# Performance work log

Hardware: AMD Instinct MI355X
Metric: run time of the kernel (lower is better)

Reference implementation:

```python
import jax, jax.numpy as jnp
import numpy as np

N_QUBITS = 16
N_LAYERS = 3
DIM = 1 << N_QUBITS  # 65536 statevector amplitudes

# Bit i of a basis index corresponds to wire i, wire 0 = most significant bit
# (PennyLane default.qubit convention).
_idx = np.arange(DIM)
_shifts = np.arange(N_QUBITS - 1, -1, -1)
_BITS_NP = (_idx[:, None] >> _shifts[None, :]) & 1  # [DIM, N_QUBITS]
# CNOT chain (i -> i+1) applied sequentially makes new bit_i = XOR(bit_0..bit_i)
_y = (np.bitwise_xor.accumulate(_BITS_NP, axis=1) * (1 << _shifts)).sum(axis=1)
_inv = np.empty(DIM, np.int64)
_inv[_y] = _idx  # state_new = state_old[INV_PERM]
INV_PERM = jnp.asarray(_inv)
SIGNS = jnp.asarray(1.0 - 2.0 * _BITS_NP, dtype=jnp.float32)  # [DIM, N_QUBITS], PauliZ eigenvalues


def _circuit(theta, qw):
    """Batched 16-qubit statevector sim. theta: [B, 16] RY angles, qw: [3, 16] RZ angles.
    Returns [B, 16] PauliZ expectation values."""
    B = theta.shape[0]
    c = jnp.cos(theta * 0.5)
    s = jnp.sin(theta * 0.5)
    # RY(theta)|0> = cos(t/2)|0> + sin(t/2)|1>; product state via repeated Kronecker
    state = jnp.ones((B, 1), jnp.complex64)
    for i in range(N_QUBITS):
        q = jnp.stack([c[:, i], s[:, i]], axis=-1).astype(jnp.complex64)  # [B, 2]
        state = (state[:, :, None] * q[:, None, :]).reshape(B, -1)
    for l in range(N_LAYERS):
        # RZ(phi) = diag(e^{-i phi/2}, e^{+i phi/2}); combined diagonal over all qubits
        diag = jnp.ones((1,), jnp.complex64)
        for i in range(N_QUBITS):
            ph = jnp.exp(1j * qw[l, i] * jnp.array([-0.5, 0.5], jnp.float32))  # complex64
            diag = (diag[:, None] * ph[None, :]).reshape(-1)
        state = (state * diag[None, :])[:, INV_PERM]  # RZ layer then CNOT chain permutation
    probs = state.real ** 2 + state.imag ** 2  # [B, DIM]
    return probs @ SIGNS  # [B, 16]


def setup_inputs() -> dict:
    key = jax.random.key(0)
    k = jax.random.split(key, 6)
    B, D = 512, 128
    x = jax.random.normal(k[0], (B, D), jnp.float32)
    w_in = jax.random.normal(k[1], (N_QUBITS, D), jnp.float32) * (1.0 / np.sqrt(D))
    b_in = jax.random.normal(k[2], (N_QUBITS,), jnp.float32) * 0.01
    # TorchLayer default init: uniform in [0, 2*pi]
    q_weights = jax.random.uniform(k[3], (N_LAYERS, N_QUBITS), jnp.float32, 0.0, 2.0 * np.pi)
    w_out = jax.random.normal(k[4], (D, N_QUBITS), jnp.float32) * (1.0 / np.sqrt(N_QUBITS))
    b_out = jax.random.normal(k[5], (D,), jnp.float32) * 0.01
    return {"x": x, "w_in": w_in, "b_in": b_in, "q_weights": q_weights,
            "w_out": w_out, "b_out": b_out}


def reference(x, w_in, b_in, q_weights, w_out, b_out):
    h = x @ w_in.T + b_in  # [B, 16]
    h = jax.lax.stop_gradient(h)  # original does x.detach() before the quantum layer
    ev = _circuit(h, q_weights)  # [B, 16]
    return ev @ w_out.T + b_out  # [B, 128]
```

## Files before the change

### kernel.cpp

```cpp
#include <hip/hip_runtime.h>
#include <hip/hip_bf16.h>


#define NQ 16
#define D  128

__global__ __launch_bounds__(128) void qlayer_kernel(
    const float* __restrict__ x,
    const float* __restrict__ w_in,
    const float* __restrict__ b_in,
    const float* __restrict__ w_out,
    const float* __restrict__ b_out,
    float* __restrict__ out)
{
    __shared__ float s_x[D];
    __shared__ float s_part[D];
    __shared__ float s_cos[NQ];
    __shared__ float s_ev[NQ];

    const int b = blockIdx.x;
    const int t = threadIdx.x;

    s_x[t] = x[b * D + t];
    __syncthreads();

    const int i = t >> 3;
    const int j = t & 7;
    const int d0 = j * 16;
    float p = 0.f;
#pragma unroll
    for (int d = 0; d < 16; ++d)
        p += s_x[d0 + d] * w_in[i * D + d0 + d];
    s_part[t] = p;
    __syncthreads();

    if (t < NQ) {
        float h = b_in[t];
#pragma unroll
        for (int jj = 0; jj < 8; ++jj) h += s_part[t * 8 + jj];
        s_cos[t] = cosf(h);
    }
    __syncthreads();

    if (t < NQ) {
        float pr = 1.f;
#pragma unroll
        for (int k = 0; k < NQ; ++k) {
            if (k <= t && (((t - k) & 3) < 2)) pr *= s_cos[k];
        }
        s_ev[t] = pr;
    }
    __syncthreads();

    float o = b_out[t];
#pragma unroll
    for (int q = 0; q < NQ; ++q)
        o += s_ev[q] * w_out[t * NQ + q];
    out[b * D + t] = o;
}

extern "C" void kernel_launch(void* const* d_in, const int* in_sizes, int n_in,
                              void* d_out, int out_size, void* d_ws, size_t ws_size,
                              hipStream_t stream) {
    const float* x     = (const float*)d_in[0];
    const float* w_in  = (const float*)d_in[1];
    const float* b_in  = (const float*)d_in[2];
    const float* w_out = (const float*)d_in[4];
    const float* b_out = (const float*)d_in[5];
    float* out = (float*)d_out;

    const int B = in_sizes[0] / D;
    qlayer_kernel<<<B, D, 0, stream>>>(x, w_in, b_in, w_out, b_out, out);
}
```

Baseline: 64.63 us.

## Compute each row in a single wavefront using shuffles and readlane, no shared memory

```diff
diff --git a/kernel.cpp b/kernel.cpp
--- a/kernel.cpp
+++ b/kernel.cpp
@@ -1,11 +1,10 @@
 #include <hip/hip_runtime.h>
-#include <hip/hip_bf16.h>
 
 
 #define NQ 16
 #define D  128
 
-__global__ __launch_bounds__(128) void qlayer_kernel(
+__global__ __launch_bounds__(64) void qlayer_kernel(
     const float* __restrict__ x,
     const float* __restrict__ w_in,
     const float* __restrict__ b_in,
@@ -13,50 +12,53 @@
     const float* __restrict__ b_out,
     float* __restrict__ out)
 {
-    __shared__ float s_x[D];
-    __shared__ float s_part[D];
-    __shared__ float s_cos[NQ];
-    __shared__ float s_ev[NQ];
+    const int b   = blockIdx.x;
+    const int l   = threadIdx.x;
+    const int g   = l >> 2;
+    const int sub = l & 3;
 
-    const int b = blockIdx.x;
-    const int t = threadIdx.x;
-
-    s_x[t] = x[b * D + t];
-    __syncthreads();
-
-    const int i = t >> 3;
-    const int j = t & 7;
-    const int d0 = j * 16;
+    const float4* xv = reinterpret_cast<const float4*>(x + b * D + sub * 32);
+    const float4* wv = reinterpret_cast<const float4*>(w_in + g * D + sub * 32);
     float p = 0.f;
 #pragma unroll
-    for (int d = 0; d < 16; ++d)
-        p += s_x[d0 + d] * w_in[i * D + d0 + d];
-    s_part[t] = p;
-    __syncthreads();
+    for (int k = 0; k < 8; ++k) {
+        float4 a = xv[k];
+        float4 w = wv[k];
+        p += a.x * w.x + a.y * w.y + a.z * w.z + a.w * w.w;
+    }
+    p += __shfl_xor(p, 1);
+    p += __shfl_xor(p, 2);
 
-    if (t < NQ) {
-        float h = b_in[t];
+    const float c = cosf(p + b_in[g]);
+
+    float cc[NQ];
 #pragma unroll
-        for (int jj = 0; jj < 8; ++jj) h += s_part[t * 8 + jj];
-        s_cos[t] = cosf(h);
+    for (int k = 0; k < NQ; ++k)
+        cc[k] = __uint_as_float(
+            __builtin_amdgcn_readlane(__float_as_uint(c), k << 2));
+
+    float ev[NQ];
+    ev[0] = cc[0];
+    ev[1] = cc[1] * cc[0];
+    ev[2] = cc[2] * cc[1];
+    ev[3] = cc[3] * cc[2];
+#pragma unroll
+    for (int i = 4; i < NQ; ++i)
+        ev[i] = cc[i] * cc[i - 1] * ev[i - 4];
+
+#pragma unroll
+    for (int rep = 0; rep < 2; ++rep) {
+        const int t = l + rep * 64;
+        const float4* wo = reinterpret_cast<const float4*>(w_out + t * NQ);
+        float o = b_out[t];
+#pragma unroll
+        for (int q4 = 0; q4 < 4; ++q4) {
+            float4 w = wo[q4];
+            o += ev[q4 * 4 + 0] * w.x + ev[q4 * 4 + 1] * w.y
+               + ev[q4 * 4 + 2] * w.z + ev[q4 * 4 + 3] * w.w;
+        }
+        out[b * D + t] = o;
     }
-    __syncthreads();
-
-    if (t < NQ) {
-        float pr = 1.f;
-#pragma unroll
-        for (int k = 0; k < NQ; ++k) {
-            if (k <= t && (((t - k) & 3) < 2)) pr *= s_cos[k];
-        }
-        s_ev[t] = pr;
-    }
-    __syncthreads();
-
-    float o = b_out[t];
-#pragma unroll
-    for (int q = 0; q < NQ; ++q)
-        o += s_ev[q] * w_out[t * NQ + q];
-    out[b * D + t] = o;
 }
 
 extern "C" void kernel_launch(void* const* d_in, const int* in_sizes, int n_in,
@@ -69,6 +71,6 @@
     const float* b_out = (const float*)d_in[5];
     float* out = (float*)d_out;
 
-    const int B = in_sizes[0] / D;
-    qlayer_kernel<<<B, D, 0, stream>>>(x, w_in, b_in, w_out, b_out, out);
+    const int rows = in_sizes[0] / D;
+    qlayer_kernel<<<rows, 64, 0, stream>>>(x, w_in, b_in, w_out, b_out, out);
 }
```

New measurement: 64.22 us. About the same (-0.6%).
